# Kernel tuning notes

Hardware: AMD Instinct MI355X
Metric: run time of the kernel (lower is better)

## Reference

```python
import jax, jax.numpy as jnp
import numpy as np

# Dimensions: N batch, Cin/Cout channels, T frames, V=25 joints, S=3 adjacency subsets
N, CIN, COUT, T, V, S = 128, 64, 64, 256, 25, 3
RED = COUT // 16            # SCE reduction channels
KER = V                     # V=25 is odd -> ker_jpt = 25, pad = 12
PAD = (KER - 1) // 2
BN_EPS = 1e-5


def setup_inputs() -> dict:
    key = jax.random.key(0)
    ks = jax.random.split(key, 12)
    x = jax.random.normal(ks[0], (N, CIN, T, V), dtype=jnp.float32)
    # fixed graph adjacency (3 subsets) and learnable PA (init: stacked identity)
    A = jax.random.uniform(ks[1], (S, V, V), dtype=jnp.float32) * (1.0 / V)
    PA = jnp.tile(jnp.eye(V, dtype=jnp.float32)[None], (S, 1, 1))
    # per-subset 1x1 conv weights [S, Cout, Cin] and biases
    wd = jax.random.normal(ks[2], (S, COUT, CIN), dtype=jnp.float32) * np.sqrt(2.0 / (COUT * S))
    bd = jnp.zeros((S, COUT), dtype=jnp.float32)
    # BatchNorm2d (inference: running stats)
    bn_gamma = jax.random.uniform(ks[3], (COUT,), dtype=jnp.float32) + 0.5
    bn_beta = jax.random.normal(ks[4], (COUT,), dtype=jnp.float32) * 0.1
    bn_mean = jax.random.normal(ks[5], (COUT,), dtype=jnp.float32) * 0.1
    bn_var = jax.random.uniform(ks[6], (COUT,), dtype=jnp.float32) + 0.5
    # SCE: conv_spatial (Conv1d Cout->RED, kernel 25, pad 12), conv_expand (1x1 RED->Cout)
    sce_ws = jax.random.normal(ks[7], (RED, COUT, KER), dtype=jnp.float32) * np.sqrt(2.0 / (COUT * KER))
    sce_bs = jnp.zeros((RED,), dtype=jnp.float32)
    sce_we = jax.random.normal(ks[8], (COUT, RED), dtype=jnp.float32) * np.sqrt(2.0 / RED)
    sce_be = jnp.zeros((COUT,), dtype=jnp.float32)
    return {"x": x, "A": A, "PA": PA, "wd": wd, "bd": bd,
            "bn_gamma": bn_gamma, "bn_beta": bn_beta, "bn_mean": bn_mean, "bn_var": bn_var,
            "sce_ws": sce_ws, "sce_bs": sce_bs, "sce_we": sce_we, "sce_be": sce_be}


def reference(x, A, PA, wd, bd, bn_gamma, bn_beta, bn_mean, bn_var,
              sce_ws, sce_bs, sce_we, sce_be):
    # L2_norm over dim=1 of PA (per subset, per column), then A = A + PA_norm
    pa_norm = jnp.sqrt(jnp.sum(PA * PA, axis=1, keepdims=True)) + 1e-4
    Af = A + PA / pa_norm                                   # [S, V, V]
    # sum_i conv1x1_i( x.view(N,CT,V) @ A[i] ): single fused contraction
    y = jnp.einsum('nctv,svw,soc->notw', x, Af, wd)
    y = y + jnp.sum(bd, axis=0)[None, :, None, None]        # [N, Cout, T, V]
    # BatchNorm2d (inference)
    scale = bn_gamma / jnp.sqrt(bn_var + BN_EPS)
    y = y * scale[None, :, None, None] + (bn_beta - bn_mean * scale)[None, :, None, None]
    # residual (in_channels == out_channels -> identity down) + ReLU
    y = jax.nn.relu(y + x)
    # SCE: temporal avg-pool -> conv1d over joints -> relu -> 1x1 expand -> sigmoid gate
    p = jnp.mean(y, axis=2)                                 # [N, Cout, V]
    s = jax.lax.conv_general_dilated(
        p, sce_ws, window_strides=(1,), padding=[(PAD, PAD)],
        dimension_numbers=('NCH', 'OIH', 'NCH')) + sce_bs[None, :, None]
    s = jax.nn.relu(s)                                      # [N, RED, V]
    g = jax.nn.sigmoid(jnp.einsum('nrv,or->nov', s, sce_we) + sce_be[None, :, None])
    # x * sigmoid(g) + x
    return y * (g[:, :, None, :] + 1.0)
```

## Files before the change

kernel.cpp:

```cpp
#include <hip/hip_runtime.h>
#include <hip/hip_bf16.h>

typedef __attribute__((ext_vector_type(8))) short short8;
typedef __attribute__((ext_vector_type(4))) short shortx4;
typedef __attribute__((ext_vector_type(4))) float floatx4;

#define NB   128
#define TT   256
#define TW   4
#define X_N  409600
#define X_C  6400

#define WS_GATE  0
#define WS_B2    204800
#define WS_AFB   204864
#define WS_W2B   206144
#define WS_PART  212288

static __device__ __forceinline__ ushort f2b(float f) {
    union { __hip_bfloat16 h; ushort u; } c;
    c.h = __float2bfloat16(f);
    return c.u;
}
static __device__ __forceinline__ float b2f(ushort u) {
    union { ushort u; __hip_bfloat16 h; } c;
    c.u = u;
    return __bfloat162float(c.h);
}

__global__ __launch_bounds__(256) void prep_kernel(
    const float* __restrict__ A, const float* __restrict__ PA,
    const float* __restrict__ wd, const float* __restrict__ bd,
    const float* __restrict__ gamma, const float* __restrict__ beta,
    const float* __restrict__ mean, const float* __restrict__ var,
    float* __restrict__ bias2, ushort* __restrict__ Afb, ushort* __restrict__ W2b)
{
    __shared__ float norms[75];
    __shared__ float scs[64];
    int tid = threadIdx.x;
    int gid = blockIdx.x * 256 + tid;
    if (tid < 75) {
        int s = tid / 25, w = tid - s * 25;
        float acc = 0.f;
        for (int i = 0; i < 25; ++i) {
            float v = PA[s * 625 + i * 25 + w];
            acc += v * v;
        }
        norms[tid] = sqrtf(acc) + 1e-4f;
    }
    if (tid < 64) {
        float sc = gamma[tid] * rsqrtf(var[tid] + 1e-5f);
        scs[tid] = sc;
        if (blockIdx.x == 0) {
            float bsum = bd[tid] + bd[64 + tid] + bd[128 + tid];
            bias2[tid] = bsum * sc + beta[tid] - mean[tid] * sc;
        }
    }
    __syncthreads();
    for (int i = gid; i < 2560; i += 4096) {
        int j = i & 7; int lane = (i >> 3) & 63; int nt = i >> 9;
        int scol = nt * 16 + (lane & 15);
        int v = ((lane >> 4) & 3) * 8 + j;
        float val = 0.f;
        if (scol < 75 && v < 25) {
            int s = scol / 25, w = scol - s * 25;
            int idx = s * 625 + v * 25 + w;
            val = A[idx] + PA[idx] / norms[s * 25 + w];
        }
        Afb[i] = f2b(val);
    }
    for (int i = gid; i < 12288; i += 4096) {
        int j = i & 7; int lane = (i >> 3) & 63; int kq = i >> 9;
        int k = kq % 6; int ot = kq / 6;
        int o = ot * 16 + (lane & 15);
        int kk = k * 32 + ((lane >> 4) & 3) * 8 + j;
        int s = kk >> 6, c = kk & 63;
        W2b[i] = f2b(wd[s * 4096 + o * 64 + c] * scs[o]);
    }
}

template<bool PART>
__global__ __launch_bounds__(512, 4) void main_kernel(
    const float* __restrict__ x, const ushort* __restrict__ Afb,
    const ushort* __restrict__ W2b, const float* __restrict__ bias2,
    float* __restrict__ yout, float* __restrict__ part)
{
    __shared__ ushort xs[4 * 64 * 36];
    __shared__ ushort zb[112 * 200];
    float* ypf = (float*)zb;

    int blk = blockIdx.x;
    int n = blk >> 6, tb = blk & 63, t0 = tb * TW;
    int tid = threadIdx.x;
    int w8 = tid >> 6, lane = tid & 63, lm = lane & 15, quad = lane >> 4;
    int ot = w8 & 3, h = w8 >> 2;

    short8 bfr[5];
    #pragma unroll
    for (int nt = 0; nt < 5; ++nt)
        bfr[nt] = *(const short8*)(Afb + (nt * 64 + lane) * 8);
    short8 wf[6];
    #pragma unroll
    for (int k = 0; k < 6; ++k)
        wf[k] = *(const short8*)(W2b + ((ot * 6 + k) * 64 + lane) * 8);
    floatx4 bias = *(const floatx4*)(bias2 + ot * 16 + quad * 4);

    const float* xn = x + (size_t)n * X_N + t0 * 25;
    for (int i = tid; i < 6400; i += 512) {
        int c = i / 100, r = i - c * 100;
        int t = r / 25, v = r - t * 25;
        xs[(t * 64 + c) * 36 + v] = f2b(xn[c * X_C + r]);
    }
    for (int i = tid; i < 1792; i += 512) {
        int c = i / 28, rr = i - c * 28;
        int t = rr / 7, v = 25 + (rr - t * 7);
        xs[(t * 64 + c) * 36 + v] = 0;
    }
    __syncthreads();

    {
        const int t = w8 & 3;
        #pragma unroll
        for (int cj = 0; cj < 2; ++cj) {
            int cm = h * 2 + cj;
            const ushort* ap = &xs[(t * 64 + cm * 16 + lm) * 36 + quad * 8];
            shortx4 a0 = *(const shortx4*)ap;
            shortx4 a1 = *(const shortx4*)(ap + 4);
            short8 av = __builtin_shufflevector(a0, a1, 0, 1, 2, 3, 4, 5, 6, 7);
            #pragma unroll
            for (int nt = 0; nt < 5; ++nt) {
                floatx4 d = __builtin_amdgcn_mfma_f32_16x16x32_bf16(
                    av, bfr[nt], (floatx4)(0.f), 0, 0, 0);
                int scol = nt * 16 + lm;
                if (scol < 75) {
                    int s = scol / 25, w = scol - s * 25;
                    int zcol = t * 25 + w;
                    int krow = s * 64 + cm * 16 + quad * 4;
                    shortx4 sv;
                    sv.x = (short)f2b(d.x); sv.y = (short)f2b(d.y);
                    sv.z = (short)f2b(d.z); sv.w = (short)f2b(d.w);
                    *(shortx4*)(&zb[zcol * 200 + krow]) = sv;
                }
            }
        }
    }
    __syncthreads();

    floatx4 acc[4];
    int nt0 = h * 4;
    #pragma unroll
    for (int j = 0; j < 4; ++j) acc[j] = bias;
    #pragma unroll
    for (int k = 0; k < 6; ++k) {
        #pragma unroll
        for (int j = 0; j < 4; ++j) {
            int nt = nt0 + j;
            if (nt < 7) {
                int col = nt * 16 + lm;
                short8 b = *(const short8*)(&zb[col * 200 + k * 32 + quad * 8]);
                acc[j] = __builtin_amdgcn_mfma_f32_16x16x32_bf16(wf[k], b, acc[j], 0, 0, 0);
            }
        }
    }
    __syncthreads();

    int o0 = ot * 16 + quad * 4;
    #pragma unroll
    for (int j = 0; j < 4; ++j) {
        int nt = nt0 + j;
        if (nt < 7) {
            int col = nt * 16 + lm;
            if (col < 100) {
                #pragma unroll
                for (int r = 0; r < 4; ++r)
                    ypf[(o0 + r) * 100 + col] = acc[j][r];
            }
        }
    }
    __syncthreads();

    size_t ybase = (size_t)n * X_N + (size_t)tb * 100;
    for (int j = tid; j < 6400; j += 512) {
        int o = j / 100, rr = j - o * 100;
        int t = rr / 25, w = rr - t * 25;
        float v = ypf[j] + b2f(xs[(t * 64 + o) * 36 + w]);
        v = fmaxf(v, 0.f);
        yout[ybase + (size_t)o * X_C + rr] = v;
        if (PART) ypf[j] = v;
    }
    if (PART) {
        __syncthreads();
        for (int i = tid; i < 1600; i += 512) {
            int o = i / 25, w = i - o * 25;
            const float* yp = &ypf[o * 100 + w];
            part[(size_t)blk * 1600 + i] = yp[0] + yp[25] + yp[50] + yp[75];
        }
    }
}

__global__ __launch_bounds__(256) void pool_kernel(
    const float* __restrict__ y, float* __restrict__ p)
{
    __shared__ float red[8][25];
    int no = blockIdx.x;
    int tid = threadIdx.x;
    if (tid < 200) {
        int tg = tid / 25, w = tid - tg * 25;
        const float* yp = y + (size_t)no * 6400 + w;
        float s = 0.f;
        for (int t = tg * 32; t < tg * 32 + 32; ++t) s += yp[t * 25];
        red[tg][w] = s;
    }
    __syncthreads();
    if (tid < 25) {
        float s = 0.f;
        #pragma unroll
        for (int g = 0; g < 8; ++g) s += red[g][tid];
        p[(size_t)no * 25 + tid] = s;
    }
}

__global__ __launch_bounds__(256) void reduce_kernel(
    const float* __restrict__ part, float* __restrict__ p)
{
    int j = blockIdx.x * 256 + threadIdx.x;
    int n = j / 1600;
    int i = j - n * 1600;
    const float* q = part + (size_t)n * 102400 + i;
    float s = 0.f;
    #pragma unroll
    for (int tb = 0; tb < 64; ++tb) s += q[tb * 1600];
    p[j] = s;
}

__global__ __launch_bounds__(256) void sce_kernel(
    const float* __restrict__ pp, const float* __restrict__ sws,
    const float* __restrict__ sbs, const float* __restrict__ swe,
    const float* __restrict__ sbe, float* __restrict__ gate)
{
    __shared__ float pm[1600];
    __shared__ float wss[6400];
    __shared__ float sq[100];
    int n = blockIdx.x, tid = threadIdx.x;
    for (int i = tid; i < 1600; i += 256)
        pm[i] = pp[(size_t)n * 1600 + i] * (1.f / 256.f);
    for (int i = tid; i < 6400; i += 256) wss[i] = sws[i];
    __syncthreads();
    if (tid < 100) {
        int r = tid / 25, w = tid - (tid / 25) * 25;
        float acc = sbs[r];
        for (int o = 0; o < 64; ++o) {
            const float* wr = &wss[(r * 64 + o) * 25];
            const float* pr = &pm[o * 25];
            int k0 = (w < 12) ? 12 - w : 0;
            int k1 = (w > 12) ? 37 - w : 25;
            for (int k = k0; k < k1; ++k) acc += pr[w + k - 12] * wr[k];
        }
        sq[tid] = fmaxf(acc, 0.f);
    }
    __syncthreads();
    for (int i = tid; i < 1600; i += 256) {
        int o = i / 25, w = i - (i / 25) * 25;
        float acc = sbe[o];
        #pragma unroll
        for (int r = 0; r < 4; ++r) acc += sq[r * 25 + w] * swe[o * 4 + r];
        gate[(size_t)n * 1600 + i] = 1.f + 1.f / (1.f + __expf(-acc));
    }
}

__global__ __launch_bounds__(320) void gate_mul_kernel(
    float* __restrict__ y, const float* __restrict__ gate)
{
    __shared__ float g100[100];
    int no = blockIdx.x;
    int tid = threadIdx.x;
    if (tid < 100) {
        int w = tid % 25;
        g100[tid] = gate[(no >> 6) * 1600 + (no & 63) * 25 + w];
    }
    __syncthreads();
    float4* yp = (float4*)(y + (size_t)no * 6400);
    #pragma unroll
    for (int it = 0; it < 5; ++it) {
        int j4 = tid + it * 320;
        float4 v = yp[j4];
        int idx = j4 % 25;
        float4 gv = *(const float4*)&g100[4 * idx];
        v.x *= gv.x; v.y *= gv.y; v.z *= gv.z; v.w *= gv.w;
        yp[j4] = v;
    }
}

extern "C" void kernel_launch(void* const* d_in, const int* in_sizes, int n_in,
                              void* d_out, int out_size, void* d_ws, size_t ws_size,
                              hipStream_t stream) {
    const float* x     = (const float*)d_in[0];
    const float* A     = (const float*)d_in[1];
    const float* PA    = (const float*)d_in[2];
    const float* wd    = (const float*)d_in[3];
    const float* bd    = (const float*)d_in[4];
    const float* gamma = (const float*)d_in[5];
    const float* beta  = (const float*)d_in[6];
    const float* mean  = (const float*)d_in[7];
    const float* var   = (const float*)d_in[8];
    const float* sws   = (const float*)d_in[9];
    const float* sbs   = (const float*)d_in[10];
    const float* swe   = (const float*)d_in[11];
    const float* sbe   = (const float*)d_in[12];

    float* out   = (float*)d_out;
    float* ws    = (float*)d_ws;
    float* gate  = ws + WS_GATE;
    float* bias2 = ws + WS_B2;
    ushort* Afb  = (ushort*)(ws + WS_AFB);
    ushort* W2b  = (ushort*)(ws + WS_W2B);
    float* part  = ws + WS_PART;

    bool useA = ws_size >= ((size_t)WS_PART + (size_t)8192 * 1600) * 4;

    prep_kernel<<<16, 256, 0, stream>>>(A, PA, wd, bd, gamma, beta, mean, var,
                                        bias2, Afb, W2b);
    if (useA) {
        main_kernel<true><<<NB * (TT / TW), 512, 0, stream>>>(x, Afb, W2b, bias2, out, part);
        reduce_kernel<<<800, 256, 0, stream>>>(part, gate);
        sce_kernel<<<NB, 256, 0, stream>>>(gate, sws, sbs, swe, sbe, gate);
    } else {
        main_kernel<false><<<NB * (TT / TW), 512, 0, stream>>>(x, Afb, W2b, bias2, out, part);
        pool_kernel<<<NB * 64, 256, 0, stream>>>(out, part);
        sce_kernel<<<NB, 256, 0, stream>>>(part, sws, sbs, swe, sbe, gate);
    }
    gate_mul_kernel<<<NB * 64, 320, 0, stream>>>(out, gate);
}
```

Measured before the change: 746.3 us.

## Shrink LDS padding for occupancy, strength-reduce index math, fold reduce into SCE

Shrinks the shared-memory x tile stride from 36 to 28 and the z buffer from 112x200 to 100x196, and raises launch bounds to 6 blocks per CU so more workgroups can be resident. The load and epilogue loops replace div/mod with incremental index updates. The separate partial-sum reduce kernel is removed and its 64-way reduction is folded into the SCE kernel, saving one launch. The new strides change LDS bank patterns and split the 16-byte B loads into two 8-byte loads, and the SCE kernel now does the reduction with only 128 blocks, which may underuse the GPU.

Result: slower. 1.242 ms (+66.5%).

```diff
diff --git a/kernel.cpp b/kernel.cpp
--- a/kernel.cpp
+++ b/kernel.cpp
@@ -80,13 +80,13 @@
 }
 
 template<bool PART>
-__global__ __launch_bounds__(512, 4) void main_kernel(
+__global__ __launch_bounds__(512, 6) void main_kernel(
     const float* __restrict__ x, const ushort* __restrict__ Afb,
     const ushort* __restrict__ W2b, const float* __restrict__ bias2,
     float* __restrict__ yout, float* __restrict__ part)
 {
-    __shared__ ushort xs[4 * 64 * 36];
-    __shared__ ushort zb[112 * 200];
+    __shared__ ushort xs[4 * 64 * 28 + 8];
+    __shared__ ushort zb[100 * 196];
     float* ypf = (float*)zb;
 
     int blk = blockIdx.x;
@@ -106,15 +106,26 @@
     floatx4 bias = *(const floatx4*)(bias2 + ot * 16 + quad * 4);
 
     const float* xn = x + (size_t)n * X_N + t0 * 25;
-    for (int i = tid; i < 6400; i += 512) {
-        int c = i / 100, r = i - c * 100;
-        int t = r / 25, v = r - t * 25;
-        xs[(t * 64 + c) * 36 + v] = f2b(xn[c * X_C + r]);
-    }
-    for (int i = tid; i < 1792; i += 512) {
-        int c = i / 28, rr = i - c * 28;
-        int t = rr / 7, v = 25 + (rr - t * 7);
-        xs[(t * 64 + c) * 36 + v] = 0;
+    {
+        int c = tid / 100;
+        int r = tid - c * 100;
+        int xoff = c * X_C + r;
+        for (int i = tid; i < 6400; i += 512) {
+            float xv = xn[xoff];
+            int t = (r * 41) >> 10;
+            int v = r - 25 * t;
+            xs[(t * 64 + c) * 28 + v] = f2b(xv);
+            int nr = r + 12;
+            int wr = (nr >= 100) ? 1 : 0;
+            r = wr ? nr - 100 : nr;
+            c += 5 + wr;
+            xoff += wr ? 38312 : 32012;
+        }
+        if (tid < 256) {
+            int b = tid * 28 + 25;
+            xs[b] = 0; xs[b + 1] = 0; xs[b + 2] = 0;
+        }
+        if (tid < 8) xs[4 * 64 * 28 + tid] = 0;
     }
     __syncthreads();
 
@@ -123,7 +134,7 @@
         #pragma unroll
         for (int cj = 0; cj < 2; ++cj) {
             int cm = h * 2 + cj;
-            const ushort* ap = &xs[(t * 64 + cm * 16 + lm) * 36 + quad * 8];
+            const ushort* ap = &xs[(t * 64 + cm * 16 + lm) * 28 + quad * 8];
             shortx4 a0 = *(const shortx4*)ap;
             shortx4 a1 = *(const shortx4*)(ap + 4);
             short8 av = __builtin_shufflevector(a0, a1, 0, 1, 2, 3, 4, 5, 6, 7);
@@ -139,7 +150,7 @@
                     shortx4 sv;
                     sv.x = (short)f2b(d.x); sv.y = (short)f2b(d.y);
                     sv.z = (short)f2b(d.z); sv.w = (short)f2b(d.w);
-                    *(shortx4*)(&zb[zcol * 200 + krow]) = sv;
+                    *(shortx4*)(&zb[zcol * 196 + krow]) = sv;
                 }
             }
         }
@@ -157,7 +168,10 @@
             int nt = nt0 + j;
             if (nt < 7) {
                 int col = nt * 16 + lm;
-                short8 b = *(const short8*)(&zb[col * 200 + k * 32 + quad * 8]);
+                const ushort* bp = &zb[col * 196 + k * 32 + quad * 8];
+                shortx4 b0 = *(const shortx4*)bp;
+                shortx4 b1 = *(const shortx4*)(bp + 4);
+                short8 b = __builtin_shufflevector(b0, b1, 0, 1, 2, 3, 4, 5, 6, 7);
                 acc[j] = __builtin_amdgcn_mfma_f32_16x16x32_bf16(wf[k], b, acc[j], 0, 0, 0);
             }
         }
@@ -180,13 +194,23 @@
     __syncthreads();
 
     size_t ybase = (size_t)n * X_N + (size_t)tb * 100;
-    for (int j = tid; j < 6400; j += 512) {
-        int o = j / 100, rr = j - o * 100;
-        int t = rr / 25, w = rr - t * 25;
-        float v = ypf[j] + b2f(xs[(t * 64 + o) * 36 + w]);
-        v = fmaxf(v, 0.f);
-        yout[ybase + (size_t)o * X_C + rr] = v;
-        if (PART) ypf[j] = v;
+    {
+        int o = tid / 100;
+        int rr = tid - o * 100;
+        int yoff = o * X_C + rr;
+        for (int j = tid; j < 6400; j += 512) {
+            int t = (rr * 41) >> 10;
+            int w = rr - 25 * t;
+            float v = ypf[j] + b2f(xs[(t * 64 + o) * 28 + w]);
+            v = fmaxf(v, 0.f);
+            yout[ybase + yoff] = v;
+            if (PART) ypf[j] = v;
+            int nr = rr + 12;
+            int wr = (nr >= 100) ? 1 : 0;
+            rr = wr ? nr - 100 : nr;
+            o += 5 + wr;
+            yoff += wr ? 38312 : 32012;
+        }
     }
     if (PART) {
         __syncthreads();
@@ -220,19 +244,7 @@
     }
 }
 
-__global__ __launch_bounds__(256) void reduce_kernel(
-    const float* __restrict__ part, float* __restrict__ p)
-{
-    int j = blockIdx.x * 256 + threadIdx.x;
-    int n = j / 1600;
-    int i = j - n * 1600;
-    const float* q = part + (size_t)n * 102400 + i;
-    float s = 0.f;
-    #pragma unroll
-    for (int tb = 0; tb < 64; ++tb) s += q[tb * 1600];
-    p[j] = s;
-}
-
+template<bool FROMPART>
 __global__ __launch_bounds__(256) void sce_kernel(
     const float* __restrict__ pp, const float* __restrict__ sws,
     const float* __restrict__ sbs, const float* __restrict__ swe,
@@ -242,8 +254,30 @@
     __shared__ float wss[6400];
     __shared__ float sq[100];
     int n = blockIdx.x, tid = threadIdx.x;
-    for (int i = tid; i < 1600; i += 256)
-        pm[i] = pp[(size_t)n * 1600 + i] * (1.f / 256.f);
+    if (FROMPART) {
+        float s0 = 0.f, s1 = 0.f, s2 = 0.f, s3 = 0.f, s4 = 0.f, s5 = 0.f, s6 = 0.f;
+        const float* q = pp + (size_t)n * 102400;
+        for (int tb = 0; tb < 64; ++tb) {
+            const float* qt = q + tb * 1600;
+            s0 += qt[tid];
+            s1 += qt[tid + 256];
+            s2 += qt[tid + 512];
+            s3 += qt[tid + 768];
+            s4 += qt[tid + 1024];
+            s5 += qt[tid + 1280];
+            if (tid < 64) s6 += qt[tid + 1536];
+        }
+        pm[tid]        = s0 * (1.f / 256.f);
+        pm[tid + 256]  = s1 * (1.f / 256.f);
+        pm[tid + 512]  = s2 * (1.f / 256.f);
+        pm[tid + 768]  = s3 * (1.f / 256.f);
+        pm[tid + 1024] = s4 * (1.f / 256.f);
+        pm[tid + 1280] = s5 * (1.f / 256.f);
+        if (tid < 64) pm[tid + 1536] = s6 * (1.f / 256.f);
+    } else {
+        for (int i = tid; i < 1600; i += 256)
+            pm[i] = pp[(size_t)n * 1600 + i] * (1.f / 256.f);
+    }
     for (int i = tid; i < 6400; i += 256) wss[i] = sws[i];
     __syncthreads();
     if (tid < 100) {
@@ -322,12 +356,11 @@
                                         bias2, Afb, W2b);
     if (useA) {
         main_kernel<true><<<NB * (TT / TW), 512, 0, stream>>>(x, Afb, W2b, bias2, out, part);
-        reduce_kernel<<<800, 256, 0, stream>>>(part, gate);
-        sce_kernel<<<NB, 256, 0, stream>>>(gate, sws, sbs, swe, sbe, gate);
+        sce_kernel<true><<<NB, 256, 0, stream>>>(part, sws, sbs, swe, sbe, gate);
     } else {
         main_kernel<false><<<NB * (TT / TW), 512, 0, stream>>>(x, Afb, W2b, bias2, out, part);
         pool_kernel<<<NB * 64, 256, 0, stream>>>(out, part);
-        sce_kernel<<<NB, 256, 0, stream>>>(part, sws, sbs, swe, sbe, gate);
+        sce_kernel<false><<<NB, 256, 0, stream>>>(part, sws, sbs, swe, sbe, gate);
     }
     gate_mul_kernel<<<NB * 64, 320, 0, stream>>>(out, gate);
 }
```
